# Optimization experiments

Hardware: AMD Instinct MI355X
Metric: run time of the kernel (lower is better)

The kernel has to match this reference:

```python
import jax, jax.numpy as jnp
import numpy as np

K = 7          # kernel_size
PAD = 3        # (dilation*(K-1)+1)//2
EPS = 1e-5     # BatchNorm eps
B, CIN, H, W = 4, 256, 56, 56
CR = 32        # rel_planes
COUT = 256     # out_planes
SP = 8         # share_planes
HN = COUT // SP  # attention heads = 32
OFFS = [(dy, dx) for dy in range(K) for dx in range(K)]


def setup_inputs() -> dict:
    key = jax.random.key(0)
    ks = jax.random.split(key, 24)
    def n(i, shape, s=0.05):
        return jax.random.normal(ks[i], shape, dtype=jnp.float32) * s
    def pos(i, shape):  # positive values for BN gamma / running var
        return jax.random.uniform(ks[i], shape, dtype=jnp.float32, minval=0.5, maxval=1.5)
    return {
        "x": jax.random.normal(ks[0], (B, CIN, H, W), dtype=jnp.float32),
        "w1c": n(1, (CR, CIN)),  "b1c": n(2, (CR,)),
        "w2c": n(3, (CR, CIN)),  "b2c": n(4, (CR,)),
        "w3c": n(5, (COUT, CIN)), "b3c": n(6, (COUT,)),
        "bn1_g": pos(7, (CR,)), "bn1_b": n(8, (CR,)), "bn1_m": n(9, (CR,)), "bn1_v": pos(10, (CR,)),
        "cw1": n(11, (CR, CR)),
        "bn2_g": pos(12, (CR,)), "bn2_b": n(13, (CR,)), "bn2_m": n(14, (CR,)), "bn2_v": pos(15, (CR,)),
        "cw2": n(16, (HN, CR)), "cw2_b": n(17, (HN,)),
    }


def _conv1x1(x, w, b):
    # x: [B,C,H,W], w: [O,C]
    return jnp.einsum('bchw,oc->bohw', x, w) + b[None, :, None, None]


def _bn(y, g, b, m, v):
    # inference BatchNorm2d over channel axis 1; y is 4D
    inv = g / jnp.sqrt(v + EPS)
    return y * inv[None, :, None, None] + (b - m * inv)[None, :, None, None]


def reference(x, w1c, b1c, w2c, b2c, w3c, b3c,
              bn1_g, bn1_b, bn1_m, bn1_v, cw1,
              bn2_g, bn2_b, bn2_m, bn2_v, cw2, cw2_b):
    x1 = _conv1x1(x, w1c, b1c)   # [B,CR,H,W]  query
    x2 = _conv1x1(x, w2c, b2c)   # [B,CR,H,W]  key
    x3 = _conv1x1(x, w3c, b3c)   # [B,COUT,H,W] value

    # Subtraction2 with reflection padding (pad_mode=1):
    # diff[b,c,k,i] = x1[b,c,i] - patch_k(x2)[b,c,i]
    x2p = jnp.pad(x2, ((0, 0), (0, 0), (PAD, PAD), (PAD, PAD)), mode='reflect')
    diff = jnp.stack([x1 - x2p[:, :, dy:dy + H, dx:dx + W] for dy, dx in OFFS],
                     axis=2)                      # [B,CR,49,H,W]
    diff = diff.reshape(B, CR, K * K, H * W)      # [B,CR,49,HW]

    # conv_w: BN -> ReLU -> 1x1 conv (no bias) -> BN -> ReLU -> 1x1 conv
    y = jax.nn.relu(_bn(diff, bn1_g, bn1_b, bn1_m, bn1_v))
    y = jnp.einsum('bkln,ok->boln', y, cw1)       # [B,CR,49,HW]
    y = jax.nn.relu(_bn(y, bn2_g, bn2_b, bn2_m, bn2_v))
    logits = jnp.einsum('bkln,ok->boln', y, cw2) + cw2_b[None, :, None, None]
    wgt = jax.nn.softmax(logits, axis=2)          # softmax over k^2, [B,HN,49,HW]
    wgt = wgt.reshape(B, HN, K * K, H, W)

    # Aggregation with reflection padding: out[b,c,i] = sum_k patch_k(x3)[b,c,i] * w[b,c//SP,k,i]
    x3p = jnp.pad(x3, ((0, 0), (0, 0), (PAD, PAD), (PAD, PAD)), mode='reflect')
    out = jnp.zeros((B, HN, SP, H, W), dtype=x.dtype)
    for k, (dy, dx) in enumerate(OFFS):
        patch = x3p[:, :, dy:dy + H, dx:dx + W].reshape(B, HN, SP, H, W)
        out = out + patch * wgt[:, :, k][:, :, None]
    return out.reshape(B, COUT, H, W)
```

## Files before the change

kernel.cpp:

```cpp
#include <hip/hip_runtime.h>
#include <math.h>

#define HW_N   3136
#define W_DIM  56
#define C_IN   256
#define C_R    32
#define C_OUT  256
#define C_ALL  320
#define K2D    49
#define RS     40
#define BN_EPS 1e-5f

typedef _Float16 h2 __attribute__((ext_vector_type(2)));
typedef __fp16  g2 __attribute__((ext_vector_type(2)));
typedef __fp16  g4 __attribute__((ext_vector_type(4)));
typedef __fp16  g8 __attribute__((ext_vector_type(8)));
typedef float   f4 __attribute__((ext_vector_type(4)));

__device__ __forceinline__ h2 pkrtz(float a, float b) {
    g2 r = __builtin_amdgcn_cvt_pkrtz(a, b);
    return __builtin_bit_cast(h2, r);
}

__device__ __forceinline__ g8 pack8(float4 a, float4 b) {
    g2 p0 = __builtin_amdgcn_cvt_pkrtz(a.x, a.y);
    g2 p1 = __builtin_amdgcn_cvt_pkrtz(a.z, a.w);
    g2 p2 = __builtin_amdgcn_cvt_pkrtz(b.x, b.y);
    g2 p3 = __builtin_amdgcn_cvt_pkrtz(b.z, b.w);
    g8 o;
    o[0] = p0[0]; o[1] = p0[1]; o[2] = p1[0]; o[3] = p1[1];
    o[4] = p2[0]; o[5] = p2[1]; o[6] = p3[0]; o[7] = p3[1];
    return o;
}

__device__ __forceinline__ int refl(int v) {
    v = (v < 0) ? -v : v;
    return (v > 55) ? (110 - v) : v;
}

__device__ __forceinline__ void wave_fence() {
    asm volatile("s_waitcnt lgkmcnt(0)" ::: "memory");
}

__global__ __launch_bounds__(256) void k_conv_mfma(
    const float* __restrict__ x,
    const float* __restrict__ w1c, const float* __restrict__ w2c,
    const float* __restrict__ w3c,
    const float* __restrict__ b1c, const float* __restrict__ b2c,
    const float* __restrict__ b3c, __fp16* __restrict__ xall16)
{
    __shared__ __align__(16) _Float16 smem[32 * 328];
    const int t = threadIdx.x, w = t >> 6, lane = t & 63;
    const int quad = lane >> 4, l16 = lane & 15;
    const int b = blockIdx.z, pos0 = blockIdx.x * 32;

    {
        const int p = t & 31;
        const int gb = t >> 5;
        const float* xp = x + (size_t)b * C_IN * HW_N + pos0 + p;
#pragma unroll
        for (int i = 0; i < 4; ++i) {
            const int g = i * 8 + gb;
            const int ci = g * 8;
            float v[8];
#pragma unroll
            for (int j = 0; j < 8; ++j) v[j] = xp[(size_t)(ci + j) * HW_N];
            g8 o;
#pragma unroll
            for (int jj = 0; jj < 4; ++jj) {
                const g2 pr = __builtin_amdgcn_cvt_pkrtz(v[2 * jj], v[2 * jj + 1]);
                o[2 * jj] = pr[0]; o[2 * jj + 1] = pr[1];
            }
            *(g8*)((__fp16*)smem + (size_t)(p * 32 + (g ^ (p & 7))) * 8) = o;
        }
    }
    __syncthreads();

    const float* wrow[5]; float bias[5];
#pragma unroll
    for (int nt = 0; nt < 5; ++nt) {
        const int co = w * 80 + nt * 16 + l16;
        wrow[nt] = (co < 32) ? (w1c + co * C_IN)
                 : (co < 64) ? (w2c + (co - 32) * C_IN)
                             : (w3c + (co - 64) * C_IN);
        bias[nt] = (co < 32) ? b1c[co] : (co < 64) ? b2c[co - 32] : b3c[co - 64];
    }

    f4 acc[2][5];
#pragma unroll
    for (int mt = 0; mt < 2; ++mt)
#pragma unroll
        for (int nt = 0; nt < 5; ++nt) acc[mt][nt] = (f4){0.f, 0.f, 0.f, 0.f};

    const int xo = l16 & 7;
#pragma unroll
    for (int ks = 0; ks < 8; ++ks) {
        g8 bf[5];
#pragma unroll
        for (int nt = 0; nt < 5; ++nt) {
            const float* wp = wrow[nt] + ks * 32 + quad * 8;
            bf[nt] = pack8(*(const float4*)wp, *(const float4*)(wp + 4));
        }
#pragma unroll
        for (int mt = 0; mt < 2; ++mt) {
            const int row = mt * 16 + l16;
            const g8 af = *(const g8*)((const __fp16*)smem
                          + (size_t)(row * 32 + ((ks * 4 + quad) ^ xo)) * 8);
#pragma unroll
            for (int nt = 0; nt < 5; ++nt)
                acc[mt][nt] = __builtin_amdgcn_mfma_f32_16x16x32_f16(af, bf[nt], acc[mt][nt], 0, 0, 0);
        }
    }
    __syncthreads();

#pragma unroll
    for (int mt = 0; mt < 2; ++mt)
#pragma unroll
        for (int nt = 0; nt < 5; ++nt) {
            const int co = w * 80 + nt * 16 + l16;
#pragma unroll
            for (int r = 0; r < 4; ++r) {
                const int row = mt * 16 + quad * 4 + r;
                smem[row * 328 + co] = (_Float16)(acc[mt][nt][r] + bias[nt]);
            }
        }
    __syncthreads();
#pragma unroll
    for (int i = 0; i < 5; ++i) {
        const int idx = i * 256 + t;
        const int row = idx / 40, c8 = idx - row * 40;
        const g8 v = *(const g8*)((const __fp16*)smem + row * 328 + c8 * 8);
        *(g8*)(xall16 + ((size_t)b * HW_N + pos0 + row) * C_ALL + c8 * 8) = v;
    }
}

__global__ __launch_bounds__(256) void k_attn(
    const __fp16* __restrict__ xq,
    const float* __restrict__ bn1_g, const float* __restrict__ bn1_b,
    const float* __restrict__ bn1_m, const float* __restrict__ bn1_v,
    const float* __restrict__ cw1,
    const float* __restrict__ bn2_g, const float* __restrict__ bn2_b,
    const float* __restrict__ bn2_m, const float* __restrict__ bn2_v,
    const float* __restrict__ cw2, const float* __restrict__ cw2_b,
    float* __restrict__ out)
{
    __shared__ __align__(16) _Float16 tbuf[4][64 * RS];
    __shared__ __align__(16) float stage[4][256];
    __shared__ int pk[4][52];
    const int tid = threadIdx.x;
    const int w = tid >> 6, lane = tid & 63;
    const int b = blockIdx.y;
    const int bid  = blockIdx.x;
    const int posb = (bid & 7) * 98 + (bid >> 3);
    const int pos0 = posb * 4;
    const int pos  = pos0 + w;
    const int y0 = pos / W_DIM, x0 = pos - y0 * W_DIM;
    const __fp16* __restrict__ base16 = xq + (size_t)b * HW_N * C_ALL;
    _Float16* tb = tbuf[w];

    {
        const int c2 = lane & 15;
        const int kh = lane >> 4;
        const float2 g = *(const float2*)(bn1_g + 2 * c2);
        const float2 bb = *(const float2*)(bn1_b + 2 * c2);
        const float2 m = *(const float2*)(bn1_m + 2 * c2);
        const float2 v = *(const float2*)(bn1_v + 2 * c2);
        const float iv0 = g.x * rsqrtf(v.x + BN_EPS), bt0 = bb.x - m.x * iv0;
        const float iv1 = g.y * rsqrtf(v.y + BN_EPS), bt1 = bb.y - m.y * iv1;
        const g2 x1p = *(const g2*)(base16 + (size_t)pos * C_ALL + 2 * c2);
        const float x1a = (float)x1p[0], x1b = (float)x1p[1];
#pragma unroll
        for (int j = 0; j < 13; ++j) {
            const int k = 4 * j + kh;
            if (k < K2D) {
                const int dy = k / 7, dx = k - dy * 7;
                const int rp = refl(y0 + dy - 3) * W_DIM + refl(x0 + dx - 3);
                if (c2 == 0) pk[w][k] = rp;
                const g2 x2p = *(const g2*)(base16 + (size_t)rp * C_ALL + 32 + 2 * c2);
                const float t0 = fmaxf((x1a - (float)x2p[0]) * iv0 + bt0, 0.f);
                const float t1 = fmaxf((x1b - (float)x2p[1]) * iv1 + bt1, 0.f);
                *(h2*)&tb[k * RS + 2 * c2] = pkrtz(t0, t1);
            }
        }
    }
    wave_fence();

    const int quad = lane >> 4, l16 = lane & 15;
    f4 acc[4][2];

    {
        g8 bf[2];
#pragma unroll
        for (int nt = 0; nt < 2; ++nt) {
            const float* wr = cw1 + (nt * 16 + l16) * C_R + quad * 8;
            bf[nt] = pack8(*(const float4*)wr, *(const float4*)(wr + 4));
        }
#pragma unroll
        for (int mt = 0; mt < 4; ++mt) {
            acc[mt][0] = (f4){0.f, 0.f, 0.f, 0.f};
            acc[mt][1] = (f4){0.f, 0.f, 0.f, 0.f};
            const g8 af = *(const g8*)((const __fp16*)tb + (mt * 16 + l16) * RS + quad * 8);
            acc[mt][0] = __builtin_amdgcn_mfma_f32_16x16x32_f16(af, bf[0], acc[mt][0], 0, 0, 0);
            acc[mt][1] = __builtin_amdgcn_mfma_f32_16x16x32_f16(af, bf[1], acc[mt][1], 0, 0, 0);
        }
    }
    wave_fence();

#pragma unroll
    for (int nt = 0; nt < 2; ++nt) {
        const int o = nt * 16 + l16;
        const float iv = bn2_g[o] * rsqrtf(bn2_v[o] + BN_EPS);
        const float bt = bn2_b[o] - bn2_m[o] * iv;
#pragma unroll
        for (int mt = 0; mt < 4; ++mt)
#pragma unroll
            for (int r = 0; r < 4; ++r) {
                const int row = mt * 16 + quad * 4 + r;
                tb[row * RS + o] = (_Float16)fmaxf(acc[mt][nt][r] * iv + bt, 0.f);
            }
    }
    wave_fence();

    {
        g8 bf[2];
#pragma unroll
        for (int nt = 0; nt < 2; ++nt) {
            const float* wr = cw2 + (nt * 16 + l16) * C_R + quad * 8;
            bf[nt] = pack8(*(const float4*)wr, *(const float4*)(wr + 4));
        }
#pragma unroll
        for (int mt = 0; mt < 4; ++mt) {
            acc[mt][0] = (f4){0.f, 0.f, 0.f, 0.f};
            acc[mt][1] = (f4){0.f, 0.f, 0.f, 0.f};
            const g8 af = *(const g8*)((const __fp16*)tb + (mt * 16 + l16) * RS + quad * 8);
            acc[mt][0] = __builtin_amdgcn_mfma_f32_16x16x32_f16(af, bf[0], acc[mt][0], 0, 0, 0);
            acc[mt][1] = __builtin_amdgcn_mfma_f32_16x16x32_f16(af, bf[1], acc[mt][1], 0, 0, 0);
        }
    }
    wave_fence();

#pragma unroll
    for (int nt = 0; nt < 2; ++nt) {
        const float bsv = cw2_b[nt * 16 + l16];
        float m = -1e30f;
#pragma unroll
        for (int mt = 0; mt < 4; ++mt)
#pragma unroll
            for (int r = 0; r < 4; ++r) {
                const int k = mt * 16 + quad * 4 + r;
                const float v = acc[mt][nt][r] + bsv;
                acc[mt][nt][r] = v;
                if (k < K2D) m = fmaxf(m, v);
            }
        m = fmaxf(m, __shfl_xor(m, 16, 64));
        m = fmaxf(m, __shfl_xor(m, 32, 64));
        float s = 0.f;
#pragma unroll
        for (int mt = 0; mt < 4; ++mt)
#pragma unroll
            for (int r = 0; r < 4; ++r) {
                const int k = mt * 16 + quad * 4 + r;
                const float e = (k < K2D) ? __expf(acc[mt][nt][r] - m) : 0.f;
                acc[mt][nt][r] = e;
                s += e;
            }
        s += __shfl_xor(s, 16, 64);
        s += __shfl_xor(s, 32, 64);
        const float rs = 1.f / s;
        const int o = nt * 16 + l16;
#pragma unroll
        for (int mt = 0; mt < 4; ++mt)
#pragma unroll
            for (int r = 0; r < 4; ++r) {
                const int row = mt * 16 + quad * 4 + r;
                tb[row * RS + o] = (_Float16)(acc[mt][nt][r] * rs);
            }
    }
    wave_fence();

    {
        const int hn = lane >> 1;
        float4 a = make_float4(0.f, 0.f, 0.f, 0.f);
#pragma unroll 7
        for (int k = 0; k < K2D; ++k) {
            const int rp = pk[w][k];
            const float wv = (float)tb[k * RS + hn];
            const g4 v = *(const g4*)(base16 + (size_t)rp * C_ALL + 64 + lane * 4);
            a.x += (float)v[0] * wv; a.y += (float)v[1] * wv;
            a.z += (float)v[2] * wv; a.w += (float)v[3] * wv;
        }
        *(float4*)&stage[w][lane * 4] = a;
    }
    __syncthreads();

    {
        const int c = tid;
        float4 o;
        o.x = stage[0][c]; o.y = stage[1][c];
        o.z = stage[2][c]; o.w = stage[3][c];
        *(float4*)(out + ((size_t)b * C_OUT + c) * HW_N + pos0) = o;
    }
}

extern "C" void kernel_launch(void* const* d_in, const int* in_sizes, int n_in,
                              void* d_out, int out_size, void* d_ws, size_t ws_size,
                              hipStream_t stream)
{
    const float* x     = (const float*)d_in[0];
    const float* w1c   = (const float*)d_in[1];
    const float* b1c   = (const float*)d_in[2];
    const float* w2c   = (const float*)d_in[3];
    const float* b2c   = (const float*)d_in[4];
    const float* w3c   = (const float*)d_in[5];
    const float* b3c   = (const float*)d_in[6];
    const float* bn1_g = (const float*)d_in[7];
    const float* bn1_b = (const float*)d_in[8];
    const float* bn1_m = (const float*)d_in[9];
    const float* bn1_v = (const float*)d_in[10];
    const float* cw1   = (const float*)d_in[11];
    const float* bn2_g = (const float*)d_in[12];
    const float* bn2_b = (const float*)d_in[13];
    const float* bn2_m = (const float*)d_in[14];
    const float* bn2_v = (const float*)d_in[15];
    const float* cw2   = (const float*)d_in[16];
    const float* cw2_b = (const float*)d_in[17];

    __fp16* xall16 = (__fp16*)d_ws;

    k_conv_mfma<<<dim3(98, 1, 4), 256, 0, stream>>>(x, w1c, w2c, w3c,
                                                    b1c, b2c, b3c, xall16);
    k_attn<<<dim3(784, 4, 1), 256, 0, stream>>>(xall16,
        bn1_g, bn1_b, bn1_m, bn1_v, cw1,
        bn2_g, bn2_b, bn2_m, bn2_v, cw2, cw2_b, (float*)d_out);
}
```

Measured before the change: 159.2 us.

## Halve conv tile to 16 positions and alias attention stage buffer into tbuf

The projection kernel now handles 16 positions per block instead of 32, doubling the grid to 784 blocks and cutting accumulators and shared memory per block, so more blocks spread across the CUs. The attention kernel drops its separate stage array and reuses the unused tail rows of each wave's tbuf, skipping softmax writes for rows past 49, to shrink LDS use and allow more resident blocks. In exchange, each weight fragment is reloaded and converted for half as many MFMAs, so weight traffic per output rises.

Result: slower. 180.5 us (+13.3%).

```diff
diff --git a/kernel.cpp b/kernel.cpp
--- a/kernel.cpp
+++ b/kernel.cpp
@@ -49,18 +49,18 @@
     const float* __restrict__ b1c, const float* __restrict__ b2c,
     const float* __restrict__ b3c, __fp16* __restrict__ xall16)
 {
-    __shared__ __align__(16) _Float16 smem[32 * 328];
+    __shared__ __align__(16) _Float16 smem[16 * 328];
     const int t = threadIdx.x, w = t >> 6, lane = t & 63;
     const int quad = lane >> 4, l16 = lane & 15;
-    const int b = blockIdx.z, pos0 = blockIdx.x * 32;
-
-    {
-        const int p = t & 31;
-        const int gb = t >> 5;
+    const int b = blockIdx.z, pos0 = blockIdx.x * 16;
+
+    {
+        const int p  = t & 15;
+        const int gb = t >> 4;
         const float* xp = x + (size_t)b * C_IN * HW_N + pos0 + p;
 #pragma unroll
-        for (int i = 0; i < 4; ++i) {
-            const int g = i * 8 + gb;
+        for (int i = 0; i < 2; ++i) {
+            const int g = i * 16 + gb;
             const int ci = g * 8;
             float v[8];
 #pragma unroll
@@ -86,51 +86,40 @@
         bias[nt] = (co < 32) ? b1c[co] : (co < 64) ? b2c[co - 32] : b3c[co - 64];
     }
 
-    f4 acc[2][5];
-#pragma unroll
-    for (int mt = 0; mt < 2; ++mt)
-#pragma unroll
-        for (int nt = 0; nt < 5; ++nt) acc[mt][nt] = (f4){0.f, 0.f, 0.f, 0.f};
+    f4 acc[5];
+#pragma unroll
+    for (int nt = 0; nt < 5; ++nt) acc[nt] = (f4){0.f, 0.f, 0.f, 0.f};
 
     const int xo = l16 & 7;
 #pragma unroll
     for (int ks = 0; ks < 8; ++ks) {
-        g8 bf[5];
+        const g8 af = *(const g8*)((const __fp16*)smem
+                      + (size_t)(l16 * 32 + ((ks * 4 + quad) ^ xo)) * 8);
 #pragma unroll
         for (int nt = 0; nt < 5; ++nt) {
             const float* wp = wrow[nt] + ks * 32 + quad * 8;
-            bf[nt] = pack8(*(const float4*)wp, *(const float4*)(wp + 4));
-        }
-#pragma unroll
-        for (int mt = 0; mt < 2; ++mt) {
-            const int row = mt * 16 + l16;
-            const g8 af = *(const g8*)((const __fp16*)smem
-                          + (size_t)(row * 32 + ((ks * 4 + quad) ^ xo)) * 8);
-#pragma unroll
-            for (int nt = 0; nt < 5; ++nt)
-                acc[mt][nt] = __builtin_amdgcn_mfma_f32_16x16x32_f16(af, bf[nt], acc[mt][nt], 0, 0, 0);
+            const g8 bf = pack8(*(const float4*)wp, *(const float4*)(wp + 4));
+            acc[nt] = __builtin_amdgcn_mfma_f32_16x16x32_f16(af, bf, acc[nt], 0, 0, 0);
         }
     }
     __syncthreads();
 
 #pragma unroll
-    for (int mt = 0; mt < 2; ++mt)
-#pragma unroll
-        for (int nt = 0; nt < 5; ++nt) {
-            const int co = w * 80 + nt * 16 + l16;
-#pragma unroll
-            for (int r = 0; r < 4; ++r) {
-                const int row = mt * 16 + quad * 4 + r;
-                smem[row * 328 + co] = (_Float16)(acc[mt][nt][r] + bias[nt]);
-            }
-        }
+    for (int nt = 0; nt < 5; ++nt) {
+        const int co = w * 80 + nt * 16 + l16;
+#pragma unroll
+        for (int r = 0; r < 4; ++r)
+            smem[(quad * 4 + r) * 328 + co] = (_Float16)(acc[nt][r] + bias[nt]);
+    }
     __syncthreads();
 #pragma unroll
-    for (int i = 0; i < 5; ++i) {
+    for (int i = 0; i < 3; ++i) {
         const int idx = i * 256 + t;
-        const int row = idx / 40, c8 = idx - row * 40;
-        const g8 v = *(const g8*)((const __fp16*)smem + row * 328 + c8 * 8);
-        *(g8*)(xall16 + ((size_t)b * HW_N + pos0 + row) * C_ALL + c8 * 8) = v;
+        if (idx < 640) {
+            const int row = idx / 40, c8 = idx - row * 40;
+            const g8 v = *(const g8*)((const __fp16*)smem + row * 328 + c8 * 8);
+            *(g8*)(xall16 + ((size_t)b * HW_N + pos0 + row) * C_ALL + c8 * 8) = v;
+        }
     }
 }
 
@@ -145,7 +134,6 @@
     float* __restrict__ out)
 {
     __shared__ __align__(16) _Float16 tbuf[4][64 * RS];
-    __shared__ __align__(16) float stage[4][256];
     __shared__ int pk[4][52];
     const int tid = threadIdx.x;
     const int w = tid >> 6, lane = tid & 63;
@@ -157,6 +145,7 @@
     const int y0 = pos / W_DIM, x0 = pos - y0 * W_DIM;
     const __fp16* __restrict__ base16 = xq + (size_t)b * HW_N * C_ALL;
     _Float16* tb = tbuf[w];
+    float* stage_w = (float*)(tb + 49 * RS);
 
     {
         const int c2 = lane & 15;
@@ -273,7 +262,8 @@
 #pragma unroll
             for (int r = 0; r < 4; ++r) {
                 const int row = mt * 16 + quad * 4 + r;
-                tb[row * RS + o] = (_Float16)(acc[mt][nt][r] * rs);
+                if (row < K2D)
+                    tb[row * RS + o] = (_Float16)(acc[mt][nt][r] * rs);
             }
     }
     wave_fence();
@@ -289,15 +279,19 @@
             a.x += (float)v[0] * wv; a.y += (float)v[1] * wv;
             a.z += (float)v[2] * wv; a.w += (float)v[3] * wv;
         }
-        *(float4*)&stage[w][lane * 4] = a;
+        *(float4*)&stage_w[lane * 4] = a;
     }
     __syncthreads();
 
     {
         const int c = tid;
+        const float* st0 = (const float*)(tbuf[0] + 49 * RS);
+        const float* st1 = (const float*)(tbuf[1] + 49 * RS);
+        const float* st2 = (const float*)(tbuf[2] + 49 * RS);
+        const float* st3 = (const float*)(tbuf[3] + 49 * RS);
         float4 o;
-        o.x = stage[0][c]; o.y = stage[1][c];
-        o.z = stage[2][c]; o.w = stage[3][c];
+        o.x = st0[c]; o.y = st1[c];
+        o.z = st2[c]; o.w = st3[c];
         *(float4*)(out + ((size_t)b * C_OUT + c) * HW_N + pos0) = o;
     }
 }
@@ -327,8 +321,8 @@
 
     __fp16* xall16 = (__fp16*)d_ws;
 
-    k_conv_mfma<<<dim3(98, 1, 4), 256, 0, stream>>>(x, w1c, w2c, w3c,
-                                                    b1c, b2c, b3c, xall16);
+    k_conv_mfma<<<dim3(196, 1, 4), 256, 0, stream>>>(x, w1c, w2c, w3c,
+                                                     b1c, b2c, b3c, xall16);
     k_attn<<<dim3(784, 4, 1), 256, 0, stream>>>(xall16,
         bn1_g, bn1_b, bn1_m, bn1_v, cw1,
         bn2_g, bn2_b, bn2_m, bn2_v, cw2, cw2_b, (float*)d_out);
```
